# Performance work log

Hardware: AMD Instinct MI355X
Metric: run time of the kernel (lower is better)

The kernel has to match this reference:

```python
import jax, jax.numpy as jnp
import numpy as np

B, N, K, D = 4, 32768, 16, 8  # batch, points, neighbors, output channels
EPS = 1e-6  # BatchNorm eps from module


def setup_inputs() -> dict:
    key = jax.random.key(0)
    ks = jax.random.split(key, 6)
    coords = jax.random.normal(ks[0], (B, N, 3), jnp.float32)
    features = jax.random.normal(ks[1], (B, D, N, 1), jnp.float32)
    knn_idx = jax.random.randint(ks[2], (B, N, K), 0, N, dtype=jnp.int64)
    knn_dist = jax.random.uniform(ks[3], (B, N, K), jnp.float32)
    mask = jnp.ones((B, N), jnp.int32)  # all-valid points
    conv_w = jax.random.normal(ks[4], (D, 10), jnp.float32) * 0.1  # 1x1 Conv2d weight (out,in)
    conv_b = jnp.zeros((D,), jnp.float32)
    bn_gamma = jnp.ones((D,), jnp.float32)
    bn_beta = jnp.zeros((D,), jnp.float32)
    return {
        "coords": coords, "features": features, "knn_idx": knn_idx,
        "knn_dist": knn_dist, "mask": mask, "conv_w": conv_w,
        "conv_b": conv_b, "bn_gamma": bn_gamma, "bn_beta": bn_beta,
    }


def reference(coords, features, knn_idx, knn_dist, mask, conv_w, conv_b, bn_gamma, bn_beta):
    # coords: (B,N,3); knn_idx/knn_dist: (B,N,K); features: (B,D,N,1); mask: (B,N)
    idx = jnp.clip(knn_idx, 0, None)
    # gather neighbor coords per batch: (B,N,K,3)
    neighbors = jax.vmap(lambda c, i: c[i])(coords, idx)
    center = jnp.broadcast_to(coords[:, :, None, :], neighbors.shape)  # (B,N,K,3)
    # masked_fill invalid points' distances with +inf (mask==0)
    dist = jnp.where(mask[:, :, None] == 0, jnp.inf, knn_dist)
    # channel-last concat: [center(3), neighbors(3), diff(3), dist(1)] -> (B,N,K,10)
    feat = jnp.concatenate(
        [center, neighbors, center - neighbors, dist[..., None]], axis=-1)
    # 1x1 conv == per-position linear 10 -> D, output layout (B,D,N,K)
    x = jnp.einsum('bnkc,dc->bdnk', feat, conv_w) + conv_b[None, :, None, None]
    # BatchNorm2d in training mode: biased batch stats over (B,N,K) per channel
    mean = x.mean(axis=(0, 2, 3), keepdims=True)
    var = x.var(axis=(0, 2, 3), keepdims=True)
    x = (x - mean) * jax.lax.rsqrt(var + EPS)
    x = x * bn_gamma[None, :, None, None] + bn_beta[None, :, None, None]
    x = jax.nn.relu(x)
    # expand features (B,D,N,1) -> (B,D,N,K) and concat on channel dim
    f = jnp.broadcast_to(features, (x.shape[0], features.shape[1], x.shape[2], x.shape[3]))
    return jnp.concatenate([x, f], axis=1)  # (B, 2D, N, K)
```

## Files before the change

### kernel.cpp

```cpp
#include <hip/hip_runtime.h>
#include <hip/hip_fp16.h>

#define NB 4
#define NP 32768
#define NK 16
#define ND 8
#define EPSV 1e-6f


__global__ __launch_bounds__(256) void lse_pass1(
    const float* __restrict__ coords,
    const float* __restrict__ features,
    const int*   __restrict__ knn_idx,
    const float* __restrict__ knn_dist,
    const int*   __restrict__ mask,
    const float* __restrict__ conv_w,
    const float* __restrict__ conv_b,
    float*       __restrict__ accum,
    __half*      __restrict__ xstage,
    float*       __restrict__ out)
{
    const int gid = blockIdx.x * 256 + threadIdx.x;
    const int b   = gid >> 17;
    const int r   = gid & (NP * 4 - 1);
    const int n   = r >> 2;
    const int k0  = (r & 3) * 4;

    float a0[ND], a1[ND], a2[ND], e0[ND], e1[ND], e2[ND], w9[ND], cb[ND];
#pragma unroll
    for (int d = 0; d < ND; ++d) {
        const float* w = conv_w + d * 10;
        float w0 = w[0], w1 = w[1], w2 = w[2];
        float w3 = w[3], w4 = w[4], w5 = w[5];
        float w6 = w[6], w7 = w[7], w8 = w[8];
        a0[d] = w0 + w6; a1[d] = w1 + w7; a2[d] = w2 + w8;
        e0[d] = w3 - w6; e1[d] = w4 - w7; e2[d] = w5 - w8;
        w9[d] = w[9];    cb[d] = conv_b[d];
    }

    const float* cbase = coords + (size_t)b * NP * 3;
    const float  cx = cbase[n * 3 + 0];
    const float  cy = cbase[n * 3 + 1];
    const float  cz = cbase[n * 3 + 2];

    const size_t p  = ((size_t)(b * NP + n)) * NK + k0;
    const int4   id = *(const int4*)(knn_idx + p);
    float4       dv = *(const float4*)(knn_dist + p);
    if (mask[b * NP + n] == 0) {
        dv.x = dv.y = dv.z = dv.w = __builtin_inff();
    }

    const int   js[4] = {id.x < 0 ? 0 : id.x, id.y < 0 ? 0 : id.y,
                         id.z < 0 ? 0 : id.z, id.w < 0 ? 0 : id.w};
    const float ds[4] = {dv.x, dv.y, dv.z, dv.w};

    float xv[4][ND];
    float sum[ND], sq[ND];
#pragma unroll
    for (int d = 0; d < ND; ++d) { sum[d] = 0.f; sq[d] = 0.f; }

#pragma unroll
    for (int t = 0; t < 4; ++t) {
        const float* nb = cbase + (size_t)js[t] * 3;
        const float  nx = nb[0], ny = nb[1], nz = nb[2];
#pragma unroll
        for (int d = 0; d < ND; ++d) {
            float x = fmaf(a0[d], cx, fmaf(a1[d], cy, fmaf(a2[d], cz,
                      fmaf(e0[d], nx, fmaf(e1[d], ny, fmaf(e2[d], nz,
                      fmaf(w9[d], ds[t], cb[d])))))));
            xv[t][d] = x;
            sum[d] += x;
            sq[d]   = fmaf(x, x, sq[d]);
        }
    }

    if (xstage) {
#pragma unroll
        for (int d = 0; d < ND; ++d) {
            __half2* o2 = (__half2*)(xstage +
                ((((size_t)(b * ND + d)) * NP + n) << 4) + k0);
            o2[0] = __floats2half2_rn(xv[0][d], xv[1][d]);
            o2[1] = __floats2half2_rn(xv[2][d], xv[3][d]);
        }
    } else {
#pragma unroll
        for (int d = 0; d < ND; ++d) {
            *(float4*)(out + ((((size_t)(b * 2 * ND + d)) * NP + n) << 4) + k0) =
                make_float4(xv[0][d], xv[1][d], xv[2][d], xv[3][d]);
        }
    }

    const float* fb = features + (size_t)b * ND * NP;
#pragma unroll
    for (int d = 0; d < ND; ++d) {
        const float v = fb[d * NP + n];
        *(float4*)(out + ((((size_t)(b * 2 * ND + ND + d)) * NP + n) << 4) + k0) =
            make_float4(v, v, v, v);
    }

#pragma unroll
    for (int d = 0; d < ND; ++d) {
        float s = sum[d], s2 = sq[d];
#pragma unroll
        for (int off = 32; off > 0; off >>= 1) {
            s  += __shfl_down(s,  off);
            s2 += __shfl_down(s2, off);
        }
        sum[d] = s; sq[d] = s2;
    }
    __shared__ float lds[4][16];
    const int wave = threadIdx.x >> 6, lane = threadIdx.x & 63;
    if (lane == 0) {
#pragma unroll
        for (int d = 0; d < ND; ++d) {
            lds[wave][d]     = sum[d];
            lds[wave][8 + d] = sq[d];
        }
    }
    __syncthreads();
    if (threadIdx.x < 16) {
        float v = lds[0][threadIdx.x] + lds[1][threadIdx.x]
                + lds[2][threadIdx.x] + lds[3][threadIdx.x];
        atomicAdd(&accum[threadIdx.x], v);
    }
}

__global__ __launch_bounds__(256) void lse_pass2(
    const float*  __restrict__ accum,
    const float*  __restrict__ bn_gamma,
    const float*  __restrict__ bn_beta,
    const __half* __restrict__ xstage,
    float*        __restrict__ out)
{
    const int    gid = blockIdx.x * 256 + threadIdx.x;
    const size_t s0  = (size_t)gid * 8;
    const int    d   = (int)((s0 >> 19) & 7);
    const int    b   = (int)(s0 >> 22);
    const size_t inp = s0 & ((1u << 19) - 1);
    const size_t o   = (((size_t)(b * 2 * ND + d)) << 19) | inp;

    const float invM = 1.0f / (float)(NB * NP * NK);
    const float mean = accum[d] * invM;
    const float var  = fmaf(-mean, mean, accum[8 + d] * invM);
    const float g    = bn_gamma[d] * rsqrtf(var + EPSV);
    const float sh   = fmaf(-mean, g, bn_beta[d]);

    float x[8];
    if (xstage) {
        const float4 raw = *(const float4*)(xstage + s0);
        const __half2* h = (const __half2*)&raw;
#pragma unroll
        for (int q = 0; q < 4; ++q) {
            float2 f = __half22float2(h[q]);
            x[2 * q]     = f.x;
            x[2 * q + 1] = f.y;
        }
    } else {
        const float4 v0 = *(const float4*)(out + o);
        const float4 v1 = *(const float4*)(out + o + 4);
        x[0] = v0.x; x[1] = v0.y; x[2] = v0.z; x[3] = v0.w;
        x[4] = v1.x; x[5] = v1.y; x[6] = v1.z; x[7] = v1.w;
    }

    float4 r0, r1;
    r0.x = fmaxf(fmaf(x[0], g, sh), 0.f);
    r0.y = fmaxf(fmaf(x[1], g, sh), 0.f);
    r0.z = fmaxf(fmaf(x[2], g, sh), 0.f);
    r0.w = fmaxf(fmaf(x[3], g, sh), 0.f);
    r1.x = fmaxf(fmaf(x[4], g, sh), 0.f);
    r1.y = fmaxf(fmaf(x[5], g, sh), 0.f);
    r1.z = fmaxf(fmaf(x[6], g, sh), 0.f);
    r1.w = fmaxf(fmaf(x[7], g, sh), 0.f);
    *(float4*)(out + o)     = r0;
    *(float4*)(out + o + 4) = r1;
}

extern "C" void kernel_launch(void* const* d_in, const int* in_sizes, int n_in,
                              void* d_out, int out_size, void* d_ws, size_t ws_size,
                              hipStream_t stream) {
    const float* coords   = (const float*)d_in[0];
    const float* features = (const float*)d_in[1];
    const int*   knn_idx  = (const int*)  d_in[2];
    const float* knn_dist = (const float*)d_in[3];
    const int*   mask     = (const int*)  d_in[4];
    const float* conv_w   = (const float*)d_in[5];
    const float* conv_b   = (const float*)d_in[6];
    const float* bn_gamma = (const float*)d_in[7];
    const float* bn_beta  = (const float*)d_in[8];
    float* out   = (float*)d_out;
    float* accum = (float*)d_ws;

    hipMemsetAsync(d_ws, 0, 64, stream);

    __half* xstage = nullptr;
    const size_t need = 256 + (size_t)NB * ND * NP * NK * sizeof(__half);
    if (ws_size >= need) xstage = (__half*)((char*)d_ws + 256);

    lse_pass1<<<(NB * NP * 4) / 256, 256, 0, stream>>>(
        coords, features, knn_idx, knn_dist, mask, conv_w, conv_b,
        accum, xstage, out);

    lse_pass2<<<(NB * ND * NP * NK / 8) / 256, 256, 0, stream>>>(
        accum, bn_gamma, bn_beta, xstage, out);
}
```

Baseline: 194.6 us.

## Recompute conv in second pass instead of staging fp16 activations

Splits the work into a stats-only kernel and a write kernel that recomputes the 1x1 conv from coords, indices and distances. The batch-norm scale and shift are folded into the conv weights and bias, so the output is written once with ReLU applied. This removes the fp16 staging buffer write and read and the separate normalize pass, at the cost of reading the indices, distances and neighbor coords twice.

```diff
diff --git a/kernel.cpp b/kernel.cpp
--- a/kernel.cpp
+++ b/kernel.cpp
@@ -1,5 +1,4 @@
 #include <hip/hip_runtime.h>
-#include <hip/hip_fp16.h>
 
 #define NB 4
 #define NP 32768
@@ -8,17 +7,14 @@
 #define EPSV 1e-6f
 
 
-__global__ __launch_bounds__(256) void lse_pass1(
+__global__ __launch_bounds__(256) void lse_stats(
     const float* __restrict__ coords,
-    const float* __restrict__ features,
     const int*   __restrict__ knn_idx,
     const float* __restrict__ knn_dist,
     const int*   __restrict__ mask,
     const float* __restrict__ conv_w,
     const float* __restrict__ conv_b,
-    float*       __restrict__ accum,
-    __half*      __restrict__ xstage,
-    float*       __restrict__ out)
+    float*       __restrict__ accum)
 {
     const int gid = blockIdx.x * 256 + threadIdx.x;
     const int b   = gid >> 17;
@@ -30,12 +26,9 @@
 #pragma unroll
     for (int d = 0; d < ND; ++d) {
         const float* w = conv_w + d * 10;
-        float w0 = w[0], w1 = w[1], w2 = w[2];
-        float w3 = w[3], w4 = w[4], w5 = w[5];
-        float w6 = w[6], w7 = w[7], w8 = w[8];
-        a0[d] = w0 + w6; a1[d] = w1 + w7; a2[d] = w2 + w8;
-        e0[d] = w3 - w6; e1[d] = w4 - w7; e2[d] = w5 - w8;
-        w9[d] = w[9];    cb[d] = conv_b[d];
+        a0[d] = w[0] + w[6]; a1[d] = w[1] + w[7]; a2[d] = w[2] + w[8];
+        e0[d] = w[3] - w[6]; e1[d] = w[4] - w[7]; e2[d] = w[5] - w[8];
+        w9[d] = w[9];        cb[d] = conv_b[d];
     }
 
     const float* cbase = coords + (size_t)b * NP * 3;
@@ -54,7 +47,6 @@
                          id.z < 0 ? 0 : id.z, id.w < 0 ? 0 : id.w};
     const float ds[4] = {dv.x, dv.y, dv.z, dv.w};
 
-    float xv[4][ND];
     float sum[ND], sq[ND];
 #pragma unroll
     for (int d = 0; d < ND; ++d) { sum[d] = 0.f; sq[d] = 0.f; }
@@ -68,34 +60,9 @@
             float x = fmaf(a0[d], cx, fmaf(a1[d], cy, fmaf(a2[d], cz,
                       fmaf(e0[d], nx, fmaf(e1[d], ny, fmaf(e2[d], nz,
                       fmaf(w9[d], ds[t], cb[d])))))));
-            xv[t][d] = x;
             sum[d] += x;
             sq[d]   = fmaf(x, x, sq[d]);
         }
-    }
-
-    if (xstage) {
-#pragma unroll
-        for (int d = 0; d < ND; ++d) {
-            __half2* o2 = (__half2*)(xstage +
-                ((((size_t)(b * ND + d)) * NP + n) << 4) + k0);
-            o2[0] = __floats2half2_rn(xv[0][d], xv[1][d]);
-            o2[1] = __floats2half2_rn(xv[2][d], xv[3][d]);
-        }
-    } else {
-#pragma unroll
-        for (int d = 0; d < ND; ++d) {
-            *(float4*)(out + ((((size_t)(b * 2 * ND + d)) * NP + n) << 4) + k0) =
-                make_float4(xv[0][d], xv[1][d], xv[2][d], xv[3][d]);
-        }
-    }
-
-    const float* fb = features + (size_t)b * ND * NP;
-#pragma unroll
-    for (int d = 0; d < ND; ++d) {
-        const float v = fb[d * NP + n];
-        *(float4*)(out + ((((size_t)(b * 2 * ND + ND + d)) * NP + n) << 4) + k0) =
-            make_float4(v, v, v, v);
     }
 
 #pragma unroll
@@ -125,54 +92,85 @@
     }
 }
 
-__global__ __launch_bounds__(256) void lse_pass2(
-    const float*  __restrict__ accum,
-    const float*  __restrict__ bn_gamma,
-    const float*  __restrict__ bn_beta,
-    const __half* __restrict__ xstage,
-    float*        __restrict__ out)
+__global__ __launch_bounds__(256) void lse_write(
+    const float* __restrict__ coords,
+    const float* __restrict__ features,
+    const int*   __restrict__ knn_idx,
+    const float* __restrict__ knn_dist,
+    const int*   __restrict__ mask,
+    const float* __restrict__ conv_w,
+    const float* __restrict__ conv_b,
+    const float* __restrict__ accum,
+    const float* __restrict__ bn_gamma,
+    const float* __restrict__ bn_beta,
+    float*       __restrict__ out)
 {
-    const int    gid = blockIdx.x * 256 + threadIdx.x;
-    const size_t s0  = (size_t)gid * 8;
-    const int    d   = (int)((s0 >> 19) & 7);
-    const int    b   = (int)(s0 >> 22);
-    const size_t inp = s0 & ((1u << 19) - 1);
-    const size_t o   = (((size_t)(b * 2 * ND + d)) << 19) | inp;
+    const int gid = blockIdx.x * 256 + threadIdx.x;
+    const int b   = gid >> 17;
+    const int r   = gid & (NP * 4 - 1);
+    const int n   = r >> 2;
+    const int k0  = (r & 3) * 4;
 
     const float invM = 1.0f / (float)(NB * NP * NK);
-    const float mean = accum[d] * invM;
-    const float var  = fmaf(-mean, mean, accum[8 + d] * invM);
-    const float g    = bn_gamma[d] * rsqrtf(var + EPSV);
-    const float sh   = fmaf(-mean, g, bn_beta[d]);
-
-    float x[8];
-    if (xstage) {
-        const float4 raw = *(const float4*)(xstage + s0);
-        const __half2* h = (const __half2*)&raw;
+    float a0[ND], a1[ND], a2[ND], e0[ND], e1[ND], e2[ND], w9[ND], cb[ND];
 #pragma unroll
-        for (int q = 0; q < 4; ++q) {
-            float2 f = __half22float2(h[q]);
-            x[2 * q]     = f.x;
-            x[2 * q + 1] = f.y;
-        }
-    } else {
-        const float4 v0 = *(const float4*)(out + o);
-        const float4 v1 = *(const float4*)(out + o + 4);
-        x[0] = v0.x; x[1] = v0.y; x[2] = v0.z; x[3] = v0.w;
-        x[4] = v1.x; x[5] = v1.y; x[6] = v1.z; x[7] = v1.w;
+    for (int d = 0; d < ND; ++d) {
+        const float* w = conv_w + d * 10;
+        const float mean = accum[d] * invM;
+        const float var  = fmaf(-mean, mean, accum[8 + d] * invM);
+        const float g    = bn_gamma[d] * rsqrtf(var + EPSV);
+        const float sh   = fmaf(-mean, g, bn_beta[d]);
+        a0[d] = (w[0] + w[6]) * g; a1[d] = (w[1] + w[7]) * g; a2[d] = (w[2] + w[8]) * g;
+        e0[d] = (w[3] - w[6]) * g; e1[d] = (w[4] - w[7]) * g; e2[d] = (w[5] - w[8]) * g;
+        w9[d] = w[9] * g;          cb[d] = fmaf(conv_b[d], g, sh);
     }
 
-    float4 r0, r1;
-    r0.x = fmaxf(fmaf(x[0], g, sh), 0.f);
-    r0.y = fmaxf(fmaf(x[1], g, sh), 0.f);
-    r0.z = fmaxf(fmaf(x[2], g, sh), 0.f);
-    r0.w = fmaxf(fmaf(x[3], g, sh), 0.f);
-    r1.x = fmaxf(fmaf(x[4], g, sh), 0.f);
-    r1.y = fmaxf(fmaf(x[5], g, sh), 0.f);
-    r1.z = fmaxf(fmaf(x[6], g, sh), 0.f);
-    r1.w = fmaxf(fmaf(x[7], g, sh), 0.f);
-    *(float4*)(out + o)     = r0;
-    *(float4*)(out + o + 4) = r1;
+    const float* cbase = coords + (size_t)b * NP * 3;
+    const float  cx = cbase[n * 3 + 0];
+    const float  cy = cbase[n * 3 + 1];
+    const float  cz = cbase[n * 3 + 2];
+
+    const size_t p  = ((size_t)(b * NP + n)) * NK + k0;
+    const int4   id = *(const int4*)(knn_idx + p);
+    float4       dv = *(const float4*)(knn_dist + p);
+    if (mask[b * NP + n] == 0) {
+        dv.x = dv.y = dv.z = dv.w = __builtin_inff();
+    }
+
+    const int   js[4] = {id.x < 0 ? 0 : id.x, id.y < 0 ? 0 : id.y,
+                         id.z < 0 ? 0 : id.z, id.w < 0 ? 0 : id.w};
+    const float ds[4] = {dv.x, dv.y, dv.z, dv.w};
+
+    float xv[4][ND];
+#pragma unroll
+    for (int t = 0; t < 4; ++t) {
+        const float* nb = cbase + (size_t)js[t] * 3;
+        const float  nx = nb[0], ny = nb[1], nz = nb[2];
+#pragma unroll
+        for (int d = 0; d < ND; ++d) {
+            xv[t][d] = fmaf(a0[d], cx, fmaf(a1[d], cy, fmaf(a2[d], cz,
+                       fmaf(e0[d], nx, fmaf(e1[d], ny, fmaf(e2[d], nz,
+                       fmaf(w9[d], ds[t], cb[d])))))));
+        }
+    }
+
+#pragma unroll
+    for (int d = 0; d < ND; ++d) {
+        float4 v;
+        v.x = fmaxf(xv[0][d], 0.f);
+        v.y = fmaxf(xv[1][d], 0.f);
+        v.z = fmaxf(xv[2][d], 0.f);
+        v.w = fmaxf(xv[3][d], 0.f);
+        *(float4*)(out + ((((size_t)(b * 2 * ND + d)) * NP + n) << 4) + k0) = v;
+    }
+
+    const float* fb = features + (size_t)b * ND * NP;
+#pragma unroll
+    for (int d = 0; d < ND; ++d) {
+        const float v = fb[d * NP + n];
+        *(float4*)(out + ((((size_t)(b * 2 * ND + ND + d)) * NP + n) << 4) + k0) =
+            make_float4(v, v, v, v);
+    }
 }
 
 extern "C" void kernel_launch(void* const* d_in, const int* in_sizes, int n_in,
@@ -192,14 +190,10 @@
 
     hipMemsetAsync(d_ws, 0, 64, stream);
 
-    __half* xstage = nullptr;
-    const size_t need = 256 + (size_t)NB * ND * NP * NK * sizeof(__half);
-    if (ws_size >= need) xstage = (__half*)((char*)d_ws + 256);
+    lse_stats<<<(NB * NP * 4) / 256, 256, 0, stream>>>(
+        coords, knn_idx, knn_dist, mask, conv_w, conv_b, accum);
 
-    lse_pass1<<<(NB * NP * 4) / 256, 256, 0, stream>>>(
+    lse_write<<<(NB * NP * 4) / 256, 256, 0, stream>>>(
         coords, features, knn_idx, knn_dist, mask, conv_w, conv_b,
-        accum, xstage, out);
-
-    lse_pass2<<<(NB * ND * NP * NK / 8) / 256, 256, 0, stream>>>(
-        accum, bn_gamma, bn_beta, xstage, out);
+        accum, bn_gamma, bn_beta, out);
 }
```

Result: slower. 213.4 us (+9.7%).
